# Optimization experiments

Measured on AMD Instinct MI355X. Metric: run time of the kernel, lower is better.

## Reference

```python
import jax, jax.numpy as jnp
import numpy as np

LEAKY_ALPHA = 0.2

def setup_inputs() -> dict:
    key = jax.random.key(0)
    kA, kH, kW, k1, k2 = jax.random.split(key, 5)
    B, N, F_in, D = 8, 2048, 256, 128
    return {
        "A": jax.random.normal(kA, (B, N, N), dtype=jnp.float32),
        "H": jax.random.normal(kH, (B, N, F_in), dtype=jnp.float32),
        "W": jax.random.normal(kW, (F_in, D), dtype=jnp.float32) * 0.05,
        "a_1": jax.random.normal(k1, (D, 1), dtype=jnp.float32) * 0.05,
        "a_2": jax.random.normal(k2, (D, 1), dtype=jnp.float32) * 0.05,
    }

def reference(A, H, W, a_1, a_2):
    # H_: [B, N, D] node projections
    H_ = jnp.einsum('bnf,fd->bnd', H, W)
    # additive attention logits: f1[b,i] + f2[b,j] -> [B, N, N]
    f1 = H_ @ a_1            # [B, N, 1]
    f2 = H_ @ a_2            # [B, N, 1]
    e = jax.nn.leaky_relu(f1 + jnp.swapaxes(f2, 1, 2), negative_slope=LEAKY_ALPHA)
    # NOTE: original multiplies logits by the binary adjacency (not -inf masking)
    mask = (A > 0.0).astype(jnp.float32)
    alpha = jax.nn.softmax(e * mask, axis=-1)   # [B, N, N]
    H_next = jnp.matmul(alpha, H_)              # [B, N, D]
    return H_next
```

## Files before the change

### kernel.cpp

```cpp
#include <hip/hip_runtime.h>


#define LEAKY 0.2f
constexpr int Bb = 8, Nn = 2048, FIN = 256, Dd = 128;
constexpr int NROW = Bb * Nn;
constexpr int RS = 132;

typedef __attribute__((ext_vector_type(8))) short short8;
typedef __attribute__((ext_vector_type(4))) float float4v;

__device__ __forceinline__ unsigned short f2bf(float f) {
    union { float f; unsigned int i; } v; v.f = f;
    return (unsigned short)((v.i + 0x8000u) >> 16);
}

__device__ __forceinline__ void stage_read(const float* __restrict__ base, int rstride,
                                           int tid, float4* st) {
    const int row = tid >> 4, c16 = tid & 15;
    const float* p = base + (size_t)row * rstride + c16 * 4;
    #pragma unroll
    for (int k = 0; k < 4; ++k) st[k] = *(const float4*)(p + 64 * k);
}
__device__ __forceinline__ void stage_write(float* __restrict__ As, int tid, const float4* st) {
    const int row = tid >> 4, c16 = tid & 15, sw = row & 7;
    float* dst = As + row * 256;
    #pragma unroll
    for (int k = 0; k < 4; ++k) {
        const int col = 4 * (c16 + 16 * k);
        dst[(col + 0) ^ sw] = st[k].x;
        dst[(col + 1) ^ sw] = st[k].y;
        dst[(col + 2) ^ sw] = st[k].z;
        dst[(col + 3) ^ sw] = st[k].w;
    }
}

__global__ __launch_bounds__(256) void prep_wf(const float* __restrict__ W,
                                               unsigned short* __restrict__ Wf) {
    int idx = blockIdx.x * 256 + threadIdx.x;
    int k = idx >> 7, d = idx & 127;
    Wf[(size_t)((k >> 3) * 128 + d) * 8 + (k & 7)] = f2bf(W[idx]);
}

__global__ __launch_bounds__(256) void proj_kernel(
    const float* __restrict__ Hg,
    const unsigned short* __restrict__ Wf,
    const float* __restrict__ a1, const float* __restrict__ a2,
    unsigned short* __restrict__ Hbt2,
    float* __restrict__ f1g, float* __restrict__ f2g) {
    __shared__ float Rbuf[4 * 16 * RS];
    __shared__ float Hs[4096];

    const int tid = threadIdx.x;
    const int w = tid >> 6, lane = tid & 63, q = lane >> 4, m = lane & 15;
    const int row0 = blockIdx.x * 16;

    float4 st[4];
    stage_read(Hg + (size_t)row0 * FIN, FIN, tid, st);
    stage_write(Hs, tid, st);
    __syncthreads();

    float4v acc[8] = {};
    const float* arow = Hs + m * 256;
    const int sw = m & 7;
    #pragma unroll
    for (int c = 0; c < 2; ++c) {
        const int cb = w * 64 + 32 * c + 8 * q;
        union { short8 v; unsigned short us[8]; } Af;
        #pragma unroll
        for (int j = 0; j < 8; ++j) Af.us[j] = f2bf(arow[cb + (j ^ sw)]);
        #pragma unroll
        for (int t = 0; t < 8; ++t) {
            const short8 bfr = *(const short8*)(Wf + (size_t)((8 * w + 4 * c + q) * 128 + 16 * t + m) * 8);
            acc[t] = __builtin_amdgcn_mfma_f32_16x16x32_bf16(Af.v, bfr, acc[t], 0, 0, 0);
        }
    }
    #pragma unroll
    for (int t = 0; t < 8; ++t)
        #pragma unroll
        for (int rg = 0; rg < 4; ++rg)
            Rbuf[w * 16 * RS + (4 * q + rg) * RS + 16 * t + m] = acc[t][rg];
    __syncthreads();

    const int row = tid >> 4, c4 = tid & 15;
    float o[8];
    #pragma unroll
    for (int half = 0; half < 2; ++half) {
        const int col = 64 * half + 4 * c4;
        const float* rb = Rbuf + row * RS + col;
        float4 s0 = *(const float4*)(rb);
        float4 s1 = *(const float4*)(rb + 16 * RS);
        float4 s2 = *(const float4*)(rb + 32 * RS);
        float4 s3 = *(const float4*)(rb + 48 * RS);
        o[4 * half + 0] = s0.x + s1.x + s2.x + s3.x;
        o[4 * half + 1] = s0.y + s1.y + s2.y + s3.y;
        o[4 * half + 2] = s0.z + s1.z + s2.z + s3.z;
        o[4 * half + 3] = s0.w + s1.w + s2.w + s3.w;
    }
    {
        float4 A1a = *(const float4*)(a1 + 4 * c4), A1b = *(const float4*)(a1 + 64 + 4 * c4);
        float4 A2a = *(const float4*)(a2 + 4 * c4), A2b = *(const float4*)(a2 + 64 + 4 * c4);
        float p1 = o[0]*A1a.x + o[1]*A1a.y + o[2]*A1a.z + o[3]*A1a.w
                 + o[4]*A1b.x + o[5]*A1b.y + o[6]*A1b.z + o[7]*A1b.w;
        float p2 = o[0]*A2a.x + o[1]*A2a.y + o[2]*A2a.z + o[3]*A2a.w
                 + o[4]*A2b.x + o[5]*A2b.y + o[6]*A2b.z + o[7]*A2b.w;
        #pragma unroll
        for (int off = 1; off <= 8; off <<= 1) {
            p1 += __shfl_xor(p1, off, 16);
            p2 += __shfl_xor(p2, off, 16);
        }
        if (c4 == 0) { f1g[row0 + row] = p1; f2g[row0 + row] = p2; }
    }
    *(float4*)(Rbuf + row * RS + 4 * c4)      = make_float4(o[0], o[1], o[2], o[3]);
    *(float4*)(Rbuf + row * RS + 64 + 4 * c4) = make_float4(o[4], o[5], o[6], o[7]);
    __syncthreads();
    const int d = tid >> 1, h = tid & 1;
    union { uint4 v; unsigned short us[8]; } oP;
    #pragma unroll
    for (int r = 0; r < 8; ++r) oP.us[r] = f2bf(Rbuf[(8 * h + r) * RS + d]);
    *(uint4*)(Hbt2 + (size_t)((2 * blockIdx.x + h) * 128 + d) * 8) = oP.v;
}

__global__ __launch_bounds__(256) void attn_kernel(
    const float* __restrict__ Ag,
    const unsigned short* __restrict__ Hbt2,
    const float* __restrict__ f1g, const float* __restrict__ f2g,
    float* __restrict__ Og) {
    __shared__ float smem[8448];
    __shared__ float f2s[2][256];
    __shared__ float Lbuf[4][16];

    const int tid = threadIdx.x;
    const int w = tid >> 6, lane = tid & 63, q = lane >> 4, m = lane & 15;
    const int b = blockIdx.y, i0 = blockIdx.x * 16;
    const size_t bRow = (size_t)b * Nn;

    const float fi = f1g[bRow + i0 + m];
    const float* Abase = Ag + (bRow + i0) * (size_t)Nn;
    const float* f2p = f2g + bRow;
    const unsigned short* Bb2 = Hbt2 + bRow * 128;
    const int jw = w * 64;

    float4v acc[8] = {};
    float lsum = 0.f;
    float4 st[4], fst;

    stage_read(Abase, Nn, tid, st);
    if (tid < 64) fst = *(const float4*)(f2p + tid * 4);
    stage_write(smem, tid, st);
    if (tid < 64) *(float4*)(&f2s[0][tid * 4]) = fst;

    for (int ch = 0; ch < 8; ++ch) {
        __syncthreads();
        const int jt = ch * 256;
        const float* As = smem + (ch & 1) * 4096;
        const float* f2c = &f2s[ch & 1][0];
        const unsigned short* bg = Bb2 + (size_t)((jt + jw) >> 3) * 1024;
        short8 bf[16];
        #pragma unroll
        for (int t = 0; t < 8; ++t) {
            bf[2 * t]     = *(const short8*)(bg + ((size_t)(q    ) * 128 + 16 * t + m) * 8);
            bf[2 * t + 1] = *(const short8*)(bg + ((size_t)(q + 4) * 128 + 16 * t + m) * 8);
        }
        __builtin_amdgcn_sched_barrier(0);
        if (ch < 7) {
            stage_read(Abase + jt + 256, Nn, tid, st);
            if (tid < 64) fst = *(const float4*)(f2p + jt + 256 + tid * 4);
        }
        __builtin_amdgcn_sched_barrier(0);
        const float* arow = As + m * 256;
        const int sw = m & 7;
        short8 pa[2];
        #pragma unroll
        for (int c = 0; c < 2; ++c) {
            const int cb = jw + 32 * c + 8 * q;
            union { short8 v; unsigned short us[8]; } P;
            #pragma unroll
            for (int j = 0; j < 8; ++j) {
                const float a = arow[cb + (j ^ sw)];
                const float s = fi + f2c[cb + j];
                float e = fmaxf(s, LEAKY * s);
                e = fminf(e, 30.f);
                const float p = (a > 0.f) ? __expf(e) : 1.0f;
                P.us[j] = f2bf(p);
                lsum += p;
            }
            pa[c] = P.v;
        }
        #pragma unroll
        for (int t = 0; t < 8; ++t) {
            acc[t] = __builtin_amdgcn_mfma_f32_16x16x32_bf16(pa[0], bf[2 * t],     acc[t], 0, 0, 0);
            acc[t] = __builtin_amdgcn_mfma_f32_16x16x32_bf16(pa[1], bf[2 * t + 1], acc[t], 0, 0, 0);
        }
        if (ch < 7) {
            stage_write(smem + ((ch + 1) & 1) * 4096, tid, st);
            if (tid < 64) *(float4*)(&f2s[(ch + 1) & 1][tid * 4]) = fst;
        }
    }

    __syncthreads();
    lsum += __shfl_xor(lsum, 16, 64);
    lsum += __shfl_xor(lsum, 32, 64);
    if (lane < 16) Lbuf[w][lane] = lsum;
    float* Rbuf = smem;
    #pragma unroll
    for (int t = 0; t < 8; ++t)
        #pragma unroll
        for (int rg = 0; rg < 4; ++rg)
            Rbuf[w * 16 * RS + (4 * q + rg) * RS + 16 * t + m] = acc[t][rg];
    __syncthreads();

    const int row = tid >> 4, c4 = tid & 15;
    float l = Lbuf[0][row] + Lbuf[1][row] + Lbuf[2][row] + Lbuf[3][row];
    float rl = 1.0f / l;
    float* orow = Og + (bRow + i0 + row) * (size_t)Dd;
    #pragma unroll
    for (int half = 0; half < 2; ++half) {
        const int col = 64 * half + 4 * c4;
        const float* rb = Rbuf + row * RS + col;
        float4 s0 = *(const float4*)(rb);
        float4 s1 = *(const float4*)(rb + 16 * RS);
        float4 s2 = *(const float4*)(rb + 32 * RS);
        float4 s3 = *(const float4*)(rb + 48 * RS);
        float4 o;
        o.x = (s0.x + s1.x + s2.x + s3.x) * rl;
        o.y = (s0.y + s1.y + s2.y + s3.y) * rl;
        o.z = (s0.z + s1.z + s2.z + s3.z) * rl;
        o.w = (s0.w + s1.w + s2.w + s3.w) * rl;
        *(float4*)(orow + col) = o;
    }
}

extern "C" void kernel_launch(void* const* d_in, const int* in_sizes, int n_in,
                              void* d_out, int out_size, void* d_ws, size_t ws_size,
                              hipStream_t stream) {
    const float* A  = (const float*)d_in[0];
    const float* H  = (const float*)d_in[1];
    const float* W  = (const float*)d_in[2];
    const float* a1 = (const float*)d_in[3];
    const float* a2 = (const float*)d_in[4];
    float* out = (float*)d_out;

    unsigned short* Wf   = (unsigned short*)d_ws;
    unsigned short* Hbt2 = Wf + FIN * Dd;
    float* f1 = (float*)(Hbt2 + (size_t)Dd * NROW);
    float* f2 = f1 + NROW;

    prep_wf<<<dim3(FIN * Dd / 256), 256, 0, stream>>>(W, Wf);
    proj_kernel<<<dim3(NROW / 16), 256, 0, stream>>>(H, Wf, a1, a2, Hbt2, f1, f2);
    attn_kernel<<<dim3(Nn / 16, Bb), 256, 0, stream>>>(A, Hbt2, f1, f2, out);
}
```

Before: 223.2 us.

## Drop W prep kernel, use exp2 with prescaled logits, compute row sums via MFMA

Removes the separate W-to-bf16 prep launch; the projection kernel now reads fp32 W directly and packs it with v_cvt_pk_bf16_f32. The f1/f2 logits are prescaled by log2(e) so the attention kernel can use raw v_exp_f32. The clamp at 30 is dropped, and bf16 packing uses the hardware pack instruction. The softmax denominator is now an extra MFMA against a ones vector instead of scalar adds and shuffles. This trims launch overhead and VALU work in the inner loop. The costs are strided fp32 W loads per block, overflow risk without the clamp, and a denominator built from bf16-rounded p values.

New measurement: 220.4 us, median of 2. About the same (-1.3%).

```diff
diff --git a/kernel.cpp b/kernel.cpp
--- a/kernel.cpp
+++ b/kernel.cpp
@@ -5,6 +5,7 @@
 constexpr int Bb = 8, Nn = 2048, FIN = 256, Dd = 128;
 constexpr int NROW = Bb * Nn;
 constexpr int RS = 132;
+constexpr float LOG2E = 1.44269504088896f;
 
 typedef __attribute__((ext_vector_type(8))) short short8;
 typedef __attribute__((ext_vector_type(4))) float float4v;
@@ -34,16 +35,9 @@
     }
 }
 
-__global__ __launch_bounds__(256) void prep_wf(const float* __restrict__ W,
-                                               unsigned short* __restrict__ Wf) {
-    int idx = blockIdx.x * 256 + threadIdx.x;
-    int k = idx >> 7, d = idx & 127;
-    Wf[(size_t)((k >> 3) * 128 + d) * 8 + (k & 7)] = f2bf(W[idx]);
-}
-
 __global__ __launch_bounds__(256) void proj_kernel(
     const float* __restrict__ Hg,
-    const unsigned short* __restrict__ Wf,
+    const float* __restrict__ Wg,
     const float* __restrict__ a1, const float* __restrict__ a2,
     unsigned short* __restrict__ Hbt2,
     float* __restrict__ f1g, float* __restrict__ f2g) {
@@ -68,10 +62,18 @@
         union { short8 v; unsigned short us[8]; } Af;
         #pragma unroll
         for (int j = 0; j < 8; ++j) Af.us[j] = f2bf(arow[cb + (j ^ sw)]);
+        const int g = 8 * w + 4 * c + q;
+        const float* wbase = Wg + (size_t)(8 * g) * 128 + m;
         #pragma unroll
         for (int t = 0; t < 8; ++t) {
-            const short8 bfr = *(const short8*)(Wf + (size_t)((8 * w + 4 * c + q) * 128 + 16 * t + m) * 8);
-            acc[t] = __builtin_amdgcn_mfma_f32_16x16x32_bf16(Af.v, bfr, acc[t], 0, 0, 0);
+            union { short8 v; unsigned int u[4]; } Bf;
+            #pragma unroll
+            for (int k2 = 0; k2 < 4; ++k2) {
+                const float lo = wbase[(2 * k2) * 128 + 16 * t];
+                const float hi = wbase[(2 * k2 + 1) * 128 + 16 * t];
+                asm("v_cvt_pk_bf16_f32 %0, %1, %2" : "=v"(Bf.u[k2]) : "v"(lo), "v"(hi));
+            }
+            acc[t] = __builtin_amdgcn_mfma_f32_16x16x32_bf16(Af.v, Bf.v, acc[t], 0, 0, 0);
         }
     }
     #pragma unroll
@@ -108,7 +110,7 @@
             p1 += __shfl_xor(p1, off, 16);
             p2 += __shfl_xor(p2, off, 16);
         }
-        if (c4 == 0) { f1g[row0 + row] = p1; f2g[row0 + row] = p2; }
+        if (c4 == 0) { f1g[row0 + row] = p1 * LOG2E; f2g[row0 + row] = p2 * LOG2E; }
     }
     *(float4*)(Rbuf + row * RS + 4 * c4)      = make_float4(o[0], o[1], o[2], o[3]);
     *(float4*)(Rbuf + row * RS + 64 + 4 * c4) = make_float4(o[4], o[5], o[6], o[7]);
@@ -127,7 +129,6 @@
     float* __restrict__ Og) {
     __shared__ float smem[8448];
     __shared__ float f2s[2][256];
-    __shared__ float Lbuf[4][16];
 
     const int tid = threadIdx.x;
     const int w = tid >> 6, lane = tid & 63, q = lane >> 4, m = lane & 15;
@@ -140,8 +141,12 @@
     const unsigned short* Bb2 = Hbt2 + bRow * 128;
     const int jw = w * 64;
 
+    short8 ones;
+    #pragma unroll
+    for (int k = 0; k < 8; ++k) ones[k] = (short)0x3F80;
+
     float4v acc[8] = {};
-    float lsum = 0.f;
+    float4v accl = {};
     float4 st[4], fst;
 
     stage_read(Abase, Nn, tid, st);
@@ -173,16 +178,21 @@
         #pragma unroll
         for (int c = 0; c < 2; ++c) {
             const int cb = jw + 32 * c + 8 * q;
-            union { short8 v; unsigned short us[8]; } P;
+            union { short8 v; unsigned int u[4]; } P;
             #pragma unroll
-            for (int j = 0; j < 8; ++j) {
-                const float a = arow[cb + (j ^ sw)];
-                const float s = fi + f2c[cb + j];
-                float e = fmaxf(s, LEAKY * s);
-                e = fminf(e, 30.f);
-                const float p = (a > 0.f) ? __expf(e) : 1.0f;
-                P.us[j] = f2bf(p);
-                lsum += p;
+            for (int k = 0; k < 4; ++k) {
+                float pv[2];
+                #pragma unroll
+                for (int hh = 0; hh < 2; ++hh) {
+                    const int j = 2 * k + hh;
+                    const float a  = arow[cb + (j ^ sw)];
+                    const float s2 = fi + f2c[cb + j];
+                    const float t2 = fmaxf(s2, LEAKY * s2);
+                    float e;
+                    asm("v_exp_f32 %0, %1" : "=v"(e) : "v"(t2));
+                    pv[hh] = (a > 0.f) ? e : 1.0f;
+                }
+                asm("v_cvt_pk_bf16_f32 %0, %1, %2" : "=v"(P.u[k]) : "v"(pv[0]), "v"(pv[1]));
             }
             pa[c] = P.v;
         }
@@ -191,6 +201,8 @@
             acc[t] = __builtin_amdgcn_mfma_f32_16x16x32_bf16(pa[0], bf[2 * t],     acc[t], 0, 0, 0);
             acc[t] = __builtin_amdgcn_mfma_f32_16x16x32_bf16(pa[1], bf[2 * t + 1], acc[t], 0, 0, 0);
         }
+        accl = __builtin_amdgcn_mfma_f32_16x16x32_bf16(pa[0], ones, accl, 0, 0, 0);
+        accl = __builtin_amdgcn_mfma_f32_16x16x32_bf16(pa[1], ones, accl, 0, 0, 0);
         if (ch < 7) {
             stage_write(smem + ((ch + 1) & 1) * 4096, tid, st);
             if (tid < 64) *(float4*)(&f2s[(ch + 1) & 1][tid * 4]) = fst;
@@ -198,20 +210,23 @@
     }
 
     __syncthreads();
-    lsum += __shfl_xor(lsum, 16, 64);
-    lsum += __shfl_xor(lsum, 32, 64);
-    if (lane < 16) Lbuf[w][lane] = lsum;
     float* Rbuf = smem;
     #pragma unroll
     for (int t = 0; t < 8; ++t)
         #pragma unroll
         for (int rg = 0; rg < 4; ++rg)
             Rbuf[w * 16 * RS + (4 * q + rg) * RS + 16 * t + m] = acc[t][rg];
+    if (m == 0) {
+        #pragma unroll
+        for (int rg = 0; rg < 4; ++rg)
+            Rbuf[w * 16 * RS + (4 * q + rg) * RS + 128] = accl[rg];
+    }
     __syncthreads();
 
     const int row = tid >> 4, c4 = tid & 15;
-    float l = Lbuf[0][row] + Lbuf[1][row] + Lbuf[2][row] + Lbuf[3][row];
-    float rl = 1.0f / l;
+    const float l = Rbuf[row * RS + 128] + Rbuf[16 * RS + row * RS + 128]
+                  + Rbuf[32 * RS + row * RS + 128] + Rbuf[48 * RS + row * RS + 128];
+    const float rl = 1.0f / l;
     float* orow = Og + (bRow + i0 + row) * (size_t)Dd;
     #pragma unroll
     for (int half = 0; half < 2; ++half) {
@@ -240,12 +255,10 @@
     const float* a2 = (const float*)d_in[4];
     float* out = (float*)d_out;
 
-    unsigned short* Wf   = (unsigned short*)d_ws;
-    unsigned short* Hbt2 = Wf + FIN * Dd;
+    unsigned short* Hbt2 = (unsigned short*)d_ws;
     float* f1 = (float*)(Hbt2 + (size_t)Dd * NROW);
     float* f2 = f1 + NROW;
 
-    prep_wf<<<dim3(FIN * Dd / 256), 256, 0, stream>>>(W, Wf);
-    proj_kernel<<<dim3(NROW / 16), 256, 0, stream>>>(H, Wf, a1, a2, Hbt2, f1, f2);
+    proj_kernel<<<dim3(NROW / 16), 256, 0, stream>>>(H, W, a1, a2, Hbt2, f1, f2);
     attn_kernel<<<dim3(Nn / 16, Bb), 256, 0, stream>>>(A, Hbt2, f1, f2, out);
 }
```
